# Kernel tuning notes

Measured on AMD Instinct MI355X. Metric: run time of the kernel, lower is better.

Reference implementation:

```python
import jax, jax.numpy as jnp
import numpy as np

VOCAB = 10000
EMBED = 512
HIDDEN = 1024
FEAT = 2048
PAD_IDX = 0


def setup_inputs() -> dict:
    key = jax.random.key(0)
    ks = jax.random.split(key, 12)
    s = lambda fan_in: 1.0 / np.sqrt(fan_in)
    features = jax.random.normal(ks[0], (64, FEAT), dtype=jnp.float32)
    captions = jax.random.randint(ks[1], (64, 32), 0, VOCAB)
    embed_table = jax.random.normal(ks[2], (VOCAB, EMBED), dtype=jnp.float32) * 0.02
    embed_table = embed_table.at[PAD_IDX].set(0.0)  # padding_idx row is zero
    W_init_h = jax.random.uniform(ks[3], (HIDDEN, FEAT), jnp.float32, -s(FEAT), s(FEAT))
    b_init_h = jnp.zeros((HIDDEN,), jnp.float32)
    W_init_c = jax.random.uniform(ks[4], (HIDDEN, FEAT), jnp.float32, -s(FEAT), s(FEAT))
    b_init_c = jnp.zeros((HIDDEN,), jnp.float32)
    W_ih = jax.random.uniform(ks[5], (4 * HIDDEN, EMBED), jnp.float32, -s(HIDDEN), s(HIDDEN))
    b_ih = jax.random.uniform(ks[6], (4 * HIDDEN,), jnp.float32, -s(HIDDEN), s(HIDDEN))
    W_hh = jax.random.uniform(ks[7], (4 * HIDDEN, HIDDEN), jnp.float32, -s(HIDDEN), s(HIDDEN))
    b_hh = jax.random.uniform(ks[8], (4 * HIDDEN,), jnp.float32, -s(HIDDEN), s(HIDDEN))
    W_fc = jax.random.uniform(ks[9], (VOCAB, HIDDEN), jnp.float32, -s(HIDDEN), s(HIDDEN))
    b_fc = jax.random.uniform(ks[10], (VOCAB,), jnp.float32, -s(HIDDEN), s(HIDDEN))
    return {
        "features": features, "captions": captions, "embed_table": embed_table,
        "W_init_h": W_init_h, "b_init_h": b_init_h, "W_init_c": W_init_c, "b_init_c": b_init_c,
        "W_ih": W_ih, "b_ih": b_ih, "W_hh": W_hh, "b_hh": b_hh,
        "W_fc": W_fc, "b_fc": b_fc,
    }


def _lstm_cell(x, h, c, W_ih, b_ih, W_hh, b_hh):
    # torch LSTMCell gate order: i, f, g, o
    gates = x @ W_ih.T + b_ih + h @ W_hh.T + b_hh  # [B, 4H]
    i, f, g, o = jnp.split(gates, 4, axis=-1)
    i = jax.nn.sigmoid(i)
    f = jax.nn.sigmoid(f)
    g = jnp.tanh(g)
    o = jax.nn.sigmoid(o)
    c = f * c + i * g
    h = o * jnp.tanh(c)
    return h, c


def reference(features, captions, embed_table, W_init_h, b_init_h, W_init_c, b_init_c,
              W_ih, b_ih, W_hh, b_hh, W_fc, b_fc):
    h0 = features @ W_init_h.T + b_init_h  # [B, H]
    c0 = features @ W_init_c.T + b_init_c  # [B, H]
    emb = embed_table[captions]            # [B, T, E]
    emb_t = jnp.swapaxes(emb, 0, 1)        # [T, B, E] for scan over time

    def step(carry, x_t):
        h, c = carry
        h, c = _lstm_cell(x_t, h, c, W_ih, b_ih, W_hh, b_hh)
        out = jax.nn.sigmoid(h @ W_fc.T + b_fc)  # [B, V]
        return (h, c), out

    _, outs = jax.lax.scan(step, (h0, c0), emb_t)
    return outs  # [T, B, V] matching torch.stack(dim=0)
```

## Files before the change

### kernel.cpp

```cpp
#include <hip/hip_runtime.h>


#define B_  64
#define T_  32
#define E_  512
#define H_  1024
#define V_  10000
#define F_  2048

typedef short short8 __attribute__((ext_vector_type(8)));
typedef float floatx4 __attribute__((ext_vector_type(4)));

__device__ __forceinline__ float bf2f(unsigned short u) {
  union { unsigned int i; float f; } c; c.i = ((unsigned int)u) << 16; return c.f;
}
__device__ __forceinline__ unsigned short f2bf(float f) {
  union { float f; unsigned int i; } c; c.f = f;
  unsigned int x = c.i;
  return (unsigned short)((x + 0x7fffu + ((x >> 16) & 1u)) >> 16);
}
__device__ __forceinline__ float sigmoidf_(float x) {
  return 1.0f / (1.0f + __expf(-x));
}
__device__ __forceinline__ void gl_lds16(const unsigned short* g, unsigned short* l) {
  __builtin_amdgcn_global_load_lds(
      (const __attribute__((address_space(1))) unsigned int*)g,
      (__attribute__((address_space(3))) unsigned int*)l, 16, 0, 0);
}
__device__ __forceinline__ int xcd_swz(int lin, int nwg) {
  if (nwg < 8) return lin;
  int q = nwg >> 3, r = nwg & 7;
  int xcd = lin & 7, pos = lin >> 3;
  return (xcd < r ? xcd * (q + 1) : r * (q + 1) + (xcd - r) * q) + pos;
}

#define C_WIH  524288
#define C_WHH  1048576
#define C_WFC  2560000
#define C_WI0  524288
#define C_WC0  524288
#define C_FEA  32768
#define C_TOT  (C_WIH + C_WHH + C_WFC + C_WI0 + C_WC0 + C_FEA)
#define NFLAGW 4096

__global__ __launch_bounds__(256) void cvt_all(
    const float* __restrict__ s0, const float* __restrict__ s1,
    const float* __restrict__ s2, const float* __restrict__ s3,
    const float* __restrict__ s4, const float* __restrict__ s5,
    unsigned short* __restrict__ d0, unsigned short* __restrict__ d1,
    unsigned short* __restrict__ d2, unsigned short* __restrict__ d3,
    unsigned short* __restrict__ d4, unsigned short* __restrict__ d5,
    unsigned int* __restrict__ flags) {
  if (blockIdx.x == 0) {
    for (int w = threadIdx.x; w < NFLAGW; w += 256) flags[w] = 0u;
  }
  int i = blockIdx.x * blockDim.x + threadIdx.x;
  int stride = gridDim.x * blockDim.x;
  for (; i < C_TOT; i += stride) {
    const float* s; unsigned short* d; int j = i;
    if (j < C_WIH)            { s = s0; d = d0; }
    else if ((j -= C_WIH) < C_WHH) { s = s1; d = d1; }
    else if ((j -= C_WHH) < C_WFC) { s = s2; d = d2; }
    else if ((j -= C_WFC) < C_WI0) { s = s3; d = d3; }
    else if ((j -= C_WI0) < C_WC0) { s = s4; d = d4; }
    else { j -= C_WC0; s = s5; d = d5; }
    float4 v = ((const float4*)s)[j];
    ushort4 o;
    o.x = f2bf(v.x); o.y = f2bf(v.y); o.z = f2bf(v.z); o.w = f2bf(v.w);
    ((ushort4*)d)[j] = o;
  }
}

__global__ __launch_bounds__(128) void embed_gather(
    const float* __restrict__ table, const int* __restrict__ captions,
    unsigned short* __restrict__ out) {
  int row = blockIdx.x;
  int t = row >> 6, b = row & 63;
  int idx = captions[b * T_ + t];
  const float4* src = (const float4*)(table + (size_t)idx * E_);
  ushort4* dst = (ushort4*)(out + (size_t)row * E_);
  for (int e = threadIdx.x; e < E_ / 4; e += blockDim.x) {
    float4 v = src[e];
    ushort4 o;
    o.x = f2bf(v.x); o.y = f2bf(v.y); o.z = f2bf(v.z); o.w = f2bf(v.w);
    dst[e] = o;
  }
}

template <int ACT_SIGMOID, int OUT_BF16, int OUT_INIT>
__global__ __launch_bounds__(256) void mfma_gemm128(
    const unsigned short* __restrict__ A, const unsigned short* __restrict__ W,
    const float* __restrict__ bias1, const float* __restrict__ bias2,
    void* __restrict__ out, void* __restrict__ out2, int M, int N, int K) {
  __shared__ unsigned short At[2][128 * 32];
  __shared__ unsigned short Wt[2][128 * 32];

  const int tid  = threadIdx.x;
  const int lane = tid & 63;
  const int wave = tid >> 6;
  const int l15  = lane & 15;
  const int quad = lane >> 4;
  const int wm   = (wave >> 1) * 64;
  const int wn   = (wave & 1) * 64;

  const int gx  = gridDim.x;
  const int nwg = gx * gridDim.y;
  const int wg  = xcd_swz(blockIdx.y * gx + blockIdx.x, nwg);
  const int m0  = (wg % gx) * 128;
  const int n0  = (wg / gx) * 128;
  const int ksl = (quad ^ (l15 & 3)) * 8;

  const int c0i = tid, c1i = tid + 256;
  const int ar0 = c0i >> 2, ak0 = (((c0i & 3) ^ (ar0 & 3)) * 8);
  const int ar1 = c1i >> 2, ak1 = (((c1i & 3) ^ (ar1 & 3)) * 8);
  int am0 = m0 + ar0; if (am0 > M - 1) am0 = M - 1;
  int am1 = m0 + ar1; if (am1 > M - 1) am1 = M - 1;
  int wn0 = n0 + ar0; if (wn0 > N - 1) wn0 = N - 1;
  int wn1 = n0 + ar1; if (wn1 > N - 1) wn1 = N - 1;
  const unsigned short* Ag0 = A + (size_t)am0 * K + ak0;
  const unsigned short* Ag1 = A + (size_t)am1 * K + ak1;
  const unsigned short* Wg0 = W + (size_t)wn0 * K + ak0;
  const unsigned short* Wg1 = W + (size_t)wn1 * K + ak1;

  floatx4 acc[4][4];
#pragma unroll
  for (int i = 0; i < 4; ++i)
#pragma unroll
    for (int j = 0; j < 4; ++j) acc[i][j] = (floatx4){0.f, 0.f, 0.f, 0.f};

  gl_lds16(Ag0, &At[0][c0i * 8]);
  gl_lds16(Ag1, &At[0][c1i * 8]);
  gl_lds16(Wg0, &Wt[0][c0i * 8]);
  gl_lds16(Wg1, &Wt[0][c1i * 8]);
  __syncthreads();

  int cur = 0;
  for (int k0 = 0; k0 < K; k0 += 32) {
    const int kn = k0 + 32;
    if (kn < K) {
      const int nb = cur ^ 1;
      gl_lds16(Ag0 + kn, &At[nb][c0i * 8]);
      gl_lds16(Ag1 + kn, &At[nb][c1i * 8]);
      gl_lds16(Wg0 + kn, &Wt[nb][c0i * 8]);
      gl_lds16(Wg1 + kn, &Wt[nb][c1i * 8]);
    }
    short8 a[4], b[4];
#pragma unroll
    for (int mt = 0; mt < 4; ++mt)
      a[mt] = *(const short8*)&At[cur][(wm + mt * 16 + l15) * 32 + ksl];
#pragma unroll
    for (int nt = 0; nt < 4; ++nt)
      b[nt] = *(const short8*)&Wt[cur][(wn + nt * 16 + l15) * 32 + ksl];
#pragma unroll
    for (int mt = 0; mt < 4; ++mt)
#pragma unroll
      for (int nt = 0; nt < 4; ++nt)
        acc[mt][nt] = __builtin_amdgcn_mfma_f32_16x16x32_bf16(a[mt], b[nt], acc[mt][nt], 0, 0, 0);
    __syncthreads();
    cur ^= 1;
  }

#pragma unroll
  for (int nt = 0; nt < 4; ++nt) {
    int col = n0 + wn + nt * 16 + l15;
    if (col >= N) continue;
    float bsum;
    if (OUT_INIT)
      bsum = (col < H_) ? bias1[col] : bias2[col - H_];
    else
      bsum = (bias1 ? bias1[col] : 0.f) + (bias2 ? bias2[col] : 0.f);
#pragma unroll
    for (int mt = 0; mt < 4; ++mt) {
#pragma unroll
      for (int r = 0; r < 4; ++r) {
        int m = m0 + wm + mt * 16 + quad * 4 + r;
        if (m >= M) continue;
        float v = acc[mt][nt][r] + bsum;
        if (ACT_SIGMOID) v = sigmoidf_(v);
        if (OUT_INIT) {
          if (col < H_)
            ((unsigned short*)out)[(size_t)m * H_ + col] = f2bf(v);
          else
            ((float*)out2)[(size_t)m * H_ + (col - H_)] = v;
        } else if (OUT_BF16) {
          ((unsigned short*)out)[(size_t)m * N + col] = f2bf(v);
        } else {
          ((float*)out)[(size_t)m * N + col] = v;
        }
      }
    }
  }
}

#define WSPAD2 1032
__global__ __launch_bounds__(512, 2) void lstm_persistent(
    const unsigned short* __restrict__ W_hh_b,
    const unsigned short* __restrict__ gx_b,
    const float* __restrict__ c0_f32,
    unsigned short* __restrict__ h_all,
    unsigned int* __restrict__ flags) {
  __shared__ unsigned short Ws[32 * WSPAD2];
  __shared__ float gbuf[4][32][33];

  const int tid  = threadIdx.x;
  const int lane = tid & 63;
  const int wave = tid >> 6;
  const int l15  = lane & 15;
  const int quad = lane >> 4;
  const int kb   = quad * 8;
  const int bid  = blockIdx.x;
  const int cg   = bid >> 1;
  const int bh   = bid & 1;
  const int colbase = cg * 8;
  const int kq   = wave >> 1;
  const int mt   = wave & 1;

#pragma unroll
  for (int it = 0; it < 8; ++it) {
    int u = wave * 8 + it;
    int n = u >> 1, half = u & 1;
    int grow = (n >> 3) * H_ + colbase + (n & 7);
    gl_lds16(W_hh_b + (size_t)grow * H_ + half * 512 + lane * 8,
             &Ws[n * WSPAD2 + half * 512]);
  }

  const int bq = tid >> 2;
  const int cp = tid & 3;
  const int gb = bh * 32 + bq;
  float cA = 0.f, cB = 0.f;
  if (tid < 128) {
    float2 cv = *(const float2*)(c0_f32 + (size_t)gb * H_ + colbase + 2 * cp);
    cA = cv.x; cB = cv.y;
  }

  const unsigned short* hbase =
      h_all + (size_t)(bh * 32 + mt * 16 + l15) * H_ + kq * 256 + kb;
  const unsigned short* wb0 = &Ws[(size_t)(l15)      * WSPAD2 + kq * 256 + kb];
  const unsigned short* wb1 = &Ws[(size_t)(16 + l15) * WSPAD2 + kq * 256 + kb];
  const unsigned int* pfw = flags + (size_t)(kq * 64 + 2 * (lane & 31) + bh);

  __syncthreads();

  for (int t = 0; t < T_; ++t) {
    unsigned int ui = 0, uf = 0, ug = 0, uo = 0;
    if (tid < 128) {
      const unsigned short* gxp =
          gx_b + (size_t)t * (B_ * 4 * H_) + (size_t)gb * (4 * H_) + colbase + 2 * cp;
      ui = *(const unsigned int*)(gxp + 0 * H_);
      uf = *(const unsigned int*)(gxp + 1 * H_);
      ug = *(const unsigned int*)(gxp + 2 * H_);
      uo = *(const unsigned int*)(gxp + 3 * H_);
    }

    if (t > 0) {
      const unsigned int tgt = (unsigned int)t;
      for (;;) {
        unsigned int v;
        asm volatile("global_load_dword %0, %1, off sc0 sc1"
                     : "=v"(v) : "v"(pfw) : "memory");
        asm volatile("s_waitcnt vmcnt(0)" ::: "memory");
        if (__all(v >= tgt)) break;
        __builtin_amdgcn_s_sleep(1);
      }
    }

    const unsigned short* hp = hbase + (size_t)t * (B_ * H_);
    short8 hx[8];
#pragma unroll
    for (int i = 0; i < 8; ++i)
      asm volatile("global_load_dwordx4 %0, %1, off sc0 sc1"
                   : "=v"(hx[i]) : "v"(hp + i * 32) : "memory");
    asm volatile("s_waitcnt vmcnt(0)" ::: "memory");
    __builtin_amdgcn_sched_barrier(0);

    floatx4 A0 = (floatx4){0.f, 0.f, 0.f, 0.f}, A1 = A0;
#pragma unroll
    for (int i = 0; i < 8; ++i) {
      short8 w0 = *(const short8*)(wb0 + i * 32);
      short8 w1 = *(const short8*)(wb1 + i * 32);
      A0 = __builtin_amdgcn_mfma_f32_16x16x32_bf16(hx[i], w0, A0, 0, 0, 0);
      A1 = __builtin_amdgcn_mfma_f32_16x16x32_bf16(hx[i], w1, A1, 0, 0, 0);
    }
#pragma unroll
    for (int r = 0; r < 4; ++r) {
      gbuf[kq][mt * 16 + quad * 4 + r][l15]      = A0[r];
      gbuf[kq][mt * 16 + quad * 4 + r][16 + l15] = A1[r];
    }
    __syncthreads();

    if (tid < 128) {
      const int c0c = 2 * cp, c1c = 2 * cp + 1;
      float giA = gbuf[0][bq][ 0 + c0c] + gbuf[1][bq][ 0 + c0c]
                + gbuf[2][bq][ 0 + c0c] + gbuf[3][bq][ 0 + c0c] + bf2f((unsigned short)(ui & 0xffff));
      float gfA = gbuf[0][bq][ 8 + c0c] + gbuf[1][bq][ 8 + c0c]
                + gbuf[2][bq][ 8 + c0c] + gbuf[3][bq][ 8 + c0c] + bf2f((unsigned short)(uf & 0xffff));
      float ggA = gbuf[0][bq][16 + c0c] + gbuf[1][bq][16 + c0c]
                + gbuf[2][bq][16 + c0c] + gbuf[3][bq][16 + c0c] + bf2f((unsigned short)(ug & 0xffff));
      float goA = gbuf[0][bq][24 + c0c] + gbuf[1][bq][24 + c0c]
                + gbuf[2][bq][24 + c0c] + gbuf[3][bq][24 + c0c] + bf2f((unsigned short)(uo & 0xffff));
      float giB = gbuf[0][bq][ 0 + c1c] + gbuf[1][bq][ 0 + c1c]
                + gbuf[2][bq][ 0 + c1c] + gbuf[3][bq][ 0 + c1c] + bf2f((unsigned short)(ui >> 16));
      float gfB = gbuf[0][bq][ 8 + c1c] + gbuf[1][bq][ 8 + c1c]
                + gbuf[2][bq][ 8 + c1c] + gbuf[3][bq][ 8 + c1c] + bf2f((unsigned short)(uf >> 16));
      float ggB = gbuf[0][bq][16 + c1c] + gbuf[1][bq][16 + c1c]
                + gbuf[2][bq][16 + c1c] + gbuf[3][bq][16 + c1c] + bf2f((unsigned short)(ug >> 16));
      float goB = gbuf[0][bq][24 + c1c] + gbuf[1][bq][24 + c1c]
                + gbuf[2][bq][24 + c1c] + gbuf[3][bq][24 + c1c] + bf2f((unsigned short)(uo >> 16));
      giA = sigmoidf_(giA); gfA = sigmoidf_(gfA); ggA = tanhf(ggA); goA = sigmoidf_(goA);
      giB = sigmoidf_(giB); gfB = sigmoidf_(gfB); ggB = tanhf(ggB); goB = sigmoidf_(goB);
      cA = gfA * cA + giA * ggA;
      cB = gfB * cB + giB * ggB;
      float hA = goA * tanhf(cA);
      float hB = goB * tanhf(cB);
      unsigned int hv = (unsigned int)f2bf(hA) | ((unsigned int)f2bf(hB) << 16);
      unsigned int* hop = (unsigned int*)(h_all + (size_t)(t + 1) * (B_ * H_)
                                          + (size_t)gb * H_ + colbase + 2 * cp);
      asm volatile("global_store_dword %0, %1, off sc0 sc1"
                   :: "v"(hop), "v"(hv) : "memory");
      asm volatile("s_waitcnt vmcnt(0)" ::: "memory");
    }

    if (t < T_ - 1) {
      __syncthreads();
      if (tid == 0) {
        const unsigned int tgt = (unsigned int)(t + 1);
        unsigned int* myf = flags + bid;
        asm volatile("global_store_dword %0, %1, off sc0 sc1"
                     :: "v"(myf), "v"(tgt) : "memory");
      }
    }
  }
}

extern "C" void kernel_launch(void* const* d_in, const int* in_sizes, int n_in,
                              void* d_out, int out_size, void* d_ws, size_t ws_size,
                              hipStream_t stream) {
  const float* features    = (const float*)d_in[0];
  const int*   captions    = (const int*)d_in[1];
  const float* embed_table = (const float*)d_in[2];
  const float* W_init_h    = (const float*)d_in[3];
  const float* b_init_h    = (const float*)d_in[4];
  const float* W_init_c    = (const float*)d_in[5];
  const float* b_init_c    = (const float*)d_in[6];
  const float* W_ih        = (const float*)d_in[7];
  const float* b_ih        = (const float*)d_in[8];
  const float* W_hh        = (const float*)d_in[9];
  const float* b_hh        = (const float*)d_in[10];
  const float* W_fc        = (const float*)d_in[11];
  const float* b_fc        = (const float*)d_in[12];
  float* out = (float*)d_out;

  char* ws = (char*)d_ws;
  auto alloc = [&](size_t bytes) -> char* {
    char* p = ws;
    ws += (bytes + 255) & ~(size_t)255;
    return p;
  };
  unsigned short* W_ih_b  = (unsigned short*)alloc((size_t)4 * H_ * E_ * 2);
  unsigned short* W_hh_b  = (unsigned short*)alloc((size_t)4 * H_ * H_ * 2);
  unsigned short* W_fc_b  = (unsigned short*)alloc((size_t)V_ * H_ * 2);
  unsigned short* Wih0_b  = (unsigned short*)alloc((size_t)H_ * F_ * 2);
  unsigned short* Wic0_b  = (unsigned short*)alloc((size_t)H_ * F_ * 2);
  unsigned short* feat_b  = (unsigned short*)alloc((size_t)B_ * F_ * 2);
  unsigned short* emb_b   = (unsigned short*)alloc((size_t)T_ * B_ * E_ * 2);
  unsigned short* gx_b    = (unsigned short*)alloc((size_t)T_ * B_ * 4 * H_ * 2);
  unsigned short* h_all   = (unsigned short*)alloc((size_t)(T_ + 1) * B_ * H_ * 2);
  float*          c_f32   = (float*)alloc((size_t)B_ * H_ * 4);
  unsigned int*   flags   = (unsigned int*)alloc((size_t)NFLAGW * 4);
  (void)ws_size; (void)in_sizes; (void)n_in; (void)out_size; (void)Wic0_b;

  hipLaunchKernelGGL(cvt_all, dim3(4096), dim3(256), 0, stream,
                     W_ih, W_hh, W_fc, W_init_h, W_init_c, features,
                     W_ih_b, W_hh_b, W_fc_b, Wih0_b, Wic0_b, feat_b, flags);

  hipLaunchKernelGGL(embed_gather, dim3(T_ * B_), dim3(128), 0, stream,
                     embed_table, captions, emb_b);

  hipLaunchKernelGGL((mfma_gemm128<0, 1, 1>), dim3(1, 2 * H_ / 128), dim3(256), 0, stream,
                     feat_b, Wih0_b, b_init_h, b_init_c,
                     (void*)h_all, (void*)c_f32, B_, 2 * H_, F_);

  hipLaunchKernelGGL((mfma_gemm128<0, 1, 0>), dim3(T_ * B_ / 128, 4 * H_ / 128), dim3(256), 0, stream,
                     emb_b, W_ih_b, b_ih, b_hh, (void*)gx_b, (void*)nullptr,
                     T_ * B_, 4 * H_, E_);

  hipLaunchKernelGGL(lstm_persistent, dim3(2 * H_ / 8), dim3(512), 0, stream,
                     W_hh_b, gx_b, c_f32, h_all, flags);

  hipLaunchKernelGGL((mfma_gemm128<1, 0, 0>), dim3(T_ * B_ / 128, (V_ + 127) / 128), dim3(256), 0, stream,
                     h_all + (size_t)B_ * H_, W_fc_b, b_fc, (const float*)nullptr,
                     (void*)out, (void*)nullptr, T_ * B_, V_, H_);
}
```

Baseline: 539.8 us.

## Fuse LSTM recurrence and output projection into one persistent producer/consumer kernel

Replaces the persistent LSTM kernel plus the separate FC GEMM with one 256-block kernel. 128 blocks run the recurrence, each covering all 64 batch rows for 8 hidden columns, so 128 blocks instead of 256 take part in each step's grid barrier. The other 128 blocks keep a swizzled 79-row slice of W_fc in LDS and compute sigmoid(h_t·W_fc^T+b) for each step once the flags show h_t is ready, overlapping the vocabulary projection with the recurrence. Flags are padded to 16-word strides and all blocks poll all 128 flags. The trade-offs are a large LDS footprint, heavy reliance on all 256 blocks being co-resident, and FC work limited to 4 waves per block.

```diff
diff --git a/kernel.cpp b/kernel.cpp
--- a/kernel.cpp
+++ b/kernel.cpp
@@ -193,140 +193,225 @@
 }
 
 #define WSPAD2 1032
-__global__ __launch_bounds__(512, 2) void lstm_persistent(
+#define SMEMB  161792
+__global__ __launch_bounds__(512, 2) void lstm_fused(
     const unsigned short* __restrict__ W_hh_b,
     const unsigned short* __restrict__ gx_b,
     const float* __restrict__ c0_f32,
     unsigned short* __restrict__ h_all,
-    unsigned int* __restrict__ flags) {
-  __shared__ unsigned short Ws[32 * WSPAD2];
-  __shared__ float gbuf[4][32][33];
+    unsigned int* __restrict__ flags,
+    const unsigned short* __restrict__ W_fc_b,
+    const float* __restrict__ b_fc,
+    float* __restrict__ out) {
+  __shared__ __align__(16) unsigned char smem[SMEMB];
 
   const int tid  = threadIdx.x;
   const int lane = tid & 63;
   const int wave = tid >> 6;
   const int l15  = lane & 15;
   const int quad = lane >> 4;
-  const int kb   = quad * 8;
   const int bid  = blockIdx.x;
-  const int cg   = bid >> 1;
-  const int bh   = bid & 1;
-  const int colbase = cg * 8;
-  const int kq   = wave >> 1;
-  const int mt   = wave & 1;
-
-#pragma unroll
-  for (int it = 0; it < 8; ++it) {
-    int u = wave * 8 + it;
-    int n = u >> 1, half = u & 1;
-    int grow = (n >> 3) * H_ + colbase + (n & 7);
-    gl_lds16(W_hh_b + (size_t)grow * H_ + half * 512 + lane * 8,
-             &Ws[n * WSPAD2 + half * 512]);
-  }
-
-  const int bq = tid >> 2;
-  const int cp = tid & 3;
-  const int gb = bh * 32 + bq;
-  float cA = 0.f, cB = 0.f;
-  if (tid < 128) {
-    float2 cv = *(const float2*)(c0_f32 + (size_t)gb * H_ + colbase + 2 * cp);
-    cA = cv.x; cB = cv.y;
-  }
-
-  const unsigned short* hbase =
-      h_all + (size_t)(bh * 32 + mt * 16 + l15) * H_ + kq * 256 + kb;
-  const unsigned short* wb0 = &Ws[(size_t)(l15)      * WSPAD2 + kq * 256 + kb];
-  const unsigned short* wb1 = &Ws[(size_t)(16 + l15) * WSPAD2 + kq * 256 + kb];
-  const unsigned int* pfw = flags + (size_t)(kq * 64 + 2 * (lane & 31) + bh);
-
+  const unsigned int* pf0 = flags + (size_t)(lane)      * 16;
+  const unsigned int* pf1 = flags + (size_t)(lane + 64) * 16;
+
+  if (bid < 128) {
+    unsigned short* Ws = (unsigned short*)smem;
+    float (*gbuf)[64][33] = (float (*)[64][33])(smem + 66048);
+    const int colbase = bid * 8;
+    const int kb  = quad * 8;
+    const int kq  = wave >> 1;
+    const int bf0 = (wave & 1) * 2;
+    const int bf1 = bf0 + 1;
+
+#pragma unroll
+    for (int it = 0; it < 8; ++it) {
+      int u = wave * 8 + it;
+      int n = u >> 1, half = u & 1;
+      int grow = (n >> 3) * H_ + colbase + (n & 7);
+      gl_lds16(W_hh_b + (size_t)grow * H_ + half * 512 + lane * 8,
+               &Ws[n * WSPAD2 + half * 512]);
+    }
+
+    const int cb = tid >> 2;
+    const int cp = tid & 3;
+    float cA = 0.f, cB = 0.f;
+    if (tid < 256) {
+      float2 cv = *(const float2*)(c0_f32 + (size_t)cb * H_ + colbase + 2 * cp);
+      cA = cv.x; cB = cv.y;
+    }
+
+    const unsigned short* hb0 = h_all + (size_t)(bf0 * 16 + l15) * H_ + kq * 256 + kb;
+    const unsigned short* hb1 = h_all + (size_t)(bf1 * 16 + l15) * H_ + kq * 256 + kb;
+    const unsigned short* wb0 = &Ws[(size_t)(l15)      * WSPAD2 + kq * 256 + kb];
+    const unsigned short* wb1 = &Ws[(size_t)(16 + l15) * WSPAD2 + kq * 256 + kb];
+
+    __syncthreads();
+
+    for (int t = 0; t < T_; ++t) {
+      unsigned int ui = 0, uf = 0, ug = 0, uo = 0;
+      if (tid < 256) {
+        const unsigned short* gxp =
+            gx_b + (size_t)t * (B_ * 4 * H_) + (size_t)cb * (4 * H_) + colbase + 2 * cp;
+        ui = *(const unsigned int*)(gxp + 0 * H_);
+        uf = *(const unsigned int*)(gxp + 1 * H_);
+        ug = *(const unsigned int*)(gxp + 2 * H_);
+        uo = *(const unsigned int*)(gxp + 3 * H_);
+      }
+
+      const size_t toff = (size_t)t * (B_ * H_);
+      short8 hx0[8], hx1[8];
+#pragma unroll
+      for (int i = 0; i < 8; ++i) {
+        asm volatile("global_load_dwordx4 %0, %1, off sc0 sc1"
+                     : "=v"(hx0[i]) : "v"(hb0 + toff + i * 32) : "memory");
+        asm volatile("global_load_dwordx4 %0, %1, off sc0 sc1"
+                     : "=v"(hx1[i]) : "v"(hb1 + toff + i * 32) : "memory");
+      }
+      asm volatile("s_waitcnt vmcnt(0)" ::: "memory");
+      __builtin_amdgcn_sched_barrier(0);
+
+      floatx4 A0 = (floatx4){0.f,0.f,0.f,0.f}, A1 = A0, B0 = A0, B1 = A0;
+#pragma unroll
+      for (int i = 0; i < 8; ++i) {
+        short8 w0 = *(const short8*)(wb0 + i * 32);
+        short8 w1 = *(const short8*)(wb1 + i * 32);
+        A0 = __builtin_amdgcn_mfma_f32_16x16x32_bf16(hx0[i], w0, A0, 0, 0, 0);
+        A1 = __builtin_amdgcn_mfma_f32_16x16x32_bf16(hx0[i], w1, A1, 0, 0, 0);
+        B0 = __builtin_amdgcn_mfma_f32_16x16x32_bf16(hx1[i], w0, B0, 0, 0, 0);
+        B1 = __builtin_amdgcn_mfma_f32_16x16x32_bf16(hx1[i], w1, B1, 0, 0, 0);
+      }
+#pragma unroll
+      for (int r = 0; r < 4; ++r) {
+        gbuf[kq][bf0 * 16 + quad * 4 + r][l15]      = A0[r];
+        gbuf[kq][bf0 * 16 + quad * 4 + r][16 + l15] = A1[r];
+        gbuf[kq][bf1 * 16 + quad * 4 + r][l15]      = B0[r];
+        gbuf[kq][bf1 * 16 + quad * 4 + r][16 + l15] = B1[r];
+      }
+      __syncthreads();
+
+      if (tid < 256) {
+        const int c0c = 2 * cp, c1c = 2 * cp + 1;
+        float giA = gbuf[0][cb][ 0 + c0c] + gbuf[1][cb][ 0 + c0c]
+                  + gbuf[2][cb][ 0 + c0c] + gbuf[3][cb][ 0 + c0c] + bf2f((unsigned short)(ui & 0xffff));
+        float gfA = gbuf[0][cb][ 8 + c0c] + gbuf[1][cb][ 8 + c0c]
+                  + gbuf[2][cb][ 8 + c0c] + gbuf[3][cb][ 8 + c0c] + bf2f((unsigned short)(uf & 0xffff));
+        float ggA = gbuf[0][cb][16 + c0c] + gbuf[1][cb][16 + c0c]
+                  + gbuf[2][cb][16 + c0c] + gbuf[3][cb][16 + c0c] + bf2f((unsigned short)(ug & 0xffff));
+        float goA = gbuf[0][cb][24 + c0c] + gbuf[1][cb][24 + c0c]
+                  + gbuf[2][cb][24 + c0c] + gbuf[3][cb][24 + c0c] + bf2f((unsigned short)(uo & 0xffff));
+        float giB = gbuf[0][cb][ 0 + c1c] + gbuf[1][cb][ 0 + c1c]
+                  + gbuf[2][cb][ 0 + c1c] + gbuf[3][cb][ 0 + c1c] + bf2f((unsigned short)(ui >> 16));
+        float gfB = gbuf[0][cb][ 8 + c1c] + gbuf[1][cb][ 8 + c1c]
+                  + gbuf[2][cb][ 8 + c1c] + gbuf[3][cb][ 8 + c1c] + bf2f((unsigned short)(uf >> 16));
+        float ggB = gbuf[0][cb][16 + c1c] + gbuf[1][cb][16 + c1c]
+                  + gbuf[2][cb][16 + c1c] + gbuf[3][cb][16 + c1c] + bf2f((unsigned short)(ug >> 16));
+        float goB = gbuf[0][cb][24 + c1c] + gbuf[1][cb][24 + c1c]
+                  + gbuf[2][cb][24 + c1c] + gbuf[3][cb][24 + c1c] + bf2f((unsigned short)(uo >> 16));
+        giA = sigmoidf_(giA); gfA = sigmoidf_(gfA); ggA = tanhf(ggA); goA = sigmoidf_(goA);
+        giB = sigmoidf_(giB); gfB = sigmoidf_(gfB); ggB = tanhf(ggB); goB = sigmoidf_(goB);
+        cA = gfA * cA + giA * ggA;
+        cB = gfB * cB + giB * ggB;
+        float hA = goA * tanhf(cA);
+        float hB = goB * tanhf(cB);
+        unsigned int hv = (unsigned int)f2bf(hA) | ((unsigned int)f2bf(hB) << 16);
+        unsigned int* hop = (unsigned int*)(h_all + (size_t)(t + 1) * (B_ * H_)
+                                            + (size_t)cb * H_ + colbase + 2 * cp);
+        asm volatile("global_store_dword %0, %1, off sc0 sc1"
+                     :: "v"(hop), "v"(hv) : "memory");
+        asm volatile("s_waitcnt vmcnt(0)" ::: "memory");
+      }
+
+      __syncthreads();
+      if (tid == 0) {
+        const unsigned int tg = (unsigned int)(t + 1);
+        unsigned int* myf = flags + (size_t)bid * 16;
+        asm volatile("global_store_dword %0, %1, off sc0 sc1"
+                     :: "v"(myf), "v"(tg) : "memory");
+      }
+      if (t < T_ - 1 && wave == 0) {
+        const unsigned int tgt = (unsigned int)(t + 1);
+        for (;;) {
+          unsigned int v0, v1;
+          asm volatile("global_load_dword %0, %1, off sc0 sc1"
+                       : "=v"(v0) : "v"(pf0) : "memory");
+          asm volatile("global_load_dword %0, %1, off sc0 sc1"
+                       : "=v"(v1) : "v"(pf1) : "memory");
+          asm volatile("s_waitcnt vmcnt(0)" ::: "memory");
+          if (__all(v0 >= tgt && v1 >= tgt)) break;
+          __builtin_amdgcn_s_sleep(1);
+        }
+      }
+      __syncthreads();
+    }
+    return;
+  }
+
+  const int f  = bid - 128;
+  const int vb = f * 79;
+  for (int it = 0; it < 20; ++it) {
+    int u = wave * 20 + it;
+    if (u < 158) {
+      int r = u >> 1, half = u & 1;
+      int vr = vb + r; if (vr > V_ - 1) vr = V_ - 1;
+      int gchunk = (half * 64 + lane) ^ (r & 7);
+      gl_lds16(W_fc_b + (size_t)vr * H_ + (size_t)gchunk * 8,
+               (unsigned short*)(smem + (size_t)r * 2048 + half * 1024));
+    }
+  }
   __syncthreads();
 
-  for (int t = 0; t < T_; ++t) {
-    unsigned int ui = 0, uf = 0, ug = 0, uo = 0;
-    if (tid < 128) {
-      const unsigned short* gxp =
-          gx_b + (size_t)t * (B_ * 4 * H_) + (size_t)gb * (4 * H_) + colbase + 2 * cp;
-      ui = *(const unsigned int*)(gxp + 0 * H_);
-      uf = *(const unsigned int*)(gxp + 1 * H_);
-      ug = *(const unsigned int*)(gxp + 2 * H_);
-      uo = *(const unsigned int*)(gxp + 3 * H_);
-    }
-
-    if (t > 0) {
+  for (int t = 1; t <= T_; ++t) {
+    if (wave == 0) {
       const unsigned int tgt = (unsigned int)t;
       for (;;) {
-        unsigned int v;
+        unsigned int v0, v1;
         asm volatile("global_load_dword %0, %1, off sc0 sc1"
-                     : "=v"(v) : "v"(pfw) : "memory");
+                     : "=v"(v0) : "v"(pf0) : "memory");
+        asm volatile("global_load_dword %0, %1, off sc0 sc1"
+                     : "=v"(v1) : "v"(pf1) : "memory");
         asm volatile("s_waitcnt vmcnt(0)" ::: "memory");
-        if (__all(v >= tgt)) break;
+        if (__all(v0 >= tgt && v1 >= tgt)) break;
         __builtin_amdgcn_s_sleep(1);
       }
     }
-
-    const unsigned short* hp = hbase + (size_t)t * (B_ * H_);
-    short8 hx[8];
-#pragma unroll
-    for (int i = 0; i < 8; ++i)
-      asm volatile("global_load_dwordx4 %0, %1, off sc0 sc1"
-                   : "=v"(hx[i]) : "v"(hp + i * 32) : "memory");
-    asm volatile("s_waitcnt vmcnt(0)" ::: "memory");
-    __builtin_amdgcn_sched_barrier(0);
-
-    floatx4 A0 = (floatx4){0.f, 0.f, 0.f, 0.f}, A1 = A0;
-#pragma unroll
-    for (int i = 0; i < 8; ++i) {
-      short8 w0 = *(const short8*)(wb0 + i * 32);
-      short8 w1 = *(const short8*)(wb1 + i * 32);
-      A0 = __builtin_amdgcn_mfma_f32_16x16x32_bf16(hx[i], w0, A0, 0, 0, 0);
-      A1 = __builtin_amdgcn_mfma_f32_16x16x32_bf16(hx[i], w1, A1, 0, 0, 0);
-    }
-#pragma unroll
-    for (int r = 0; r < 4; ++r) {
-      gbuf[kq][mt * 16 + quad * 4 + r][l15]      = A0[r];
-      gbuf[kq][mt * 16 + quad * 4 + r][16 + l15] = A1[r];
-    }
     __syncthreads();
 
-    if (tid < 128) {
-      const int c0c = 2 * cp, c1c = 2 * cp + 1;
-      float giA = gbuf[0][bq][ 0 + c0c] + gbuf[1][bq][ 0 + c0c]
-                + gbuf[2][bq][ 0 + c0c] + gbuf[3][bq][ 0 + c0c] + bf2f((unsigned short)(ui & 0xffff));
-      float gfA = gbuf[0][bq][ 8 + c0c] + gbuf[1][bq][ 8 + c0c]
-                + gbuf[2][bq][ 8 + c0c] + gbuf[3][bq][ 8 + c0c] + bf2f((unsigned short)(uf & 0xffff));
-      float ggA = gbuf[0][bq][16 + c0c] + gbuf[1][bq][16 + c0c]
-                + gbuf[2][bq][16 + c0c] + gbuf[3][bq][16 + c0c] + bf2f((unsigned short)(ug & 0xffff));
-      float goA = gbuf[0][bq][24 + c0c] + gbuf[1][bq][24 + c0c]
-                + gbuf[2][bq][24 + c0c] + gbuf[3][bq][24 + c0c] + bf2f((unsigned short)(uo & 0xffff));
-      float giB = gbuf[0][bq][ 0 + c1c] + gbuf[1][bq][ 0 + c1c]
-                + gbuf[2][bq][ 0 + c1c] + gbuf[3][bq][ 0 + c1c] + bf2f((unsigned short)(ui >> 16));
-      float gfB = gbuf[0][bq][ 8 + c1c] + gbuf[1][bq][ 8 + c1c]
-                + gbuf[2][bq][ 8 + c1c] + gbuf[3][bq][ 8 + c1c] + bf2f((unsigned short)(uf >> 16));
-      float ggB = gbuf[0][bq][16 + c1c] + gbuf[1][bq][16 + c1c]
-                + gbuf[2][bq][16 + c1c] + gbuf[3][bq][16 + c1c] + bf2f((unsigned short)(ug >> 16));
-      float goB = gbuf[0][bq][24 + c1c] + gbuf[1][bq][24 + c1c]
-                + gbuf[2][bq][24 + c1c] + gbuf[3][bq][24 + c1c] + bf2f((unsigned short)(uo >> 16));
-      giA = sigmoidf_(giA); gfA = sigmoidf_(gfA); ggA = tanhf(ggA); goA = sigmoidf_(goA);
-      giB = sigmoidf_(giB); gfB = sigmoidf_(gfB); ggB = tanhf(ggB); goB = sigmoidf_(goB);
-      cA = gfA * cA + giA * ggA;
-      cB = gfB * cB + giB * ggB;
-      float hA = goA * tanhf(cA);
-      float hB = goB * tanhf(cB);
-      unsigned int hv = (unsigned int)f2bf(hA) | ((unsigned int)f2bf(hB) << 16);
-      unsigned int* hop = (unsigned int*)(h_all + (size_t)(t + 1) * (B_ * H_)
-                                          + (size_t)gb * H_ + colbase + 2 * cp);
-      asm volatile("global_store_dword %0, %1, off sc0 sc1"
-                   :: "v"(hop), "v"(hv) : "memory");
-      asm volatile("s_waitcnt vmcnt(0)" ::: "memory");
-    }
-
-    if (t < T_ - 1) {
-      __syncthreads();
-      if (tid == 0) {
-        const unsigned int tgt = (unsigned int)(t + 1);
-        unsigned int* myf = flags + bid;
-        asm volatile("global_store_dword %0, %1, off sc0 sc1"
-                     :: "v"(myf), "v"(tgt) : "memory");
+    if (wave >= 1 && wave <= 4) {
+      const int bf = wave - 1;
+      const unsigned short* ap =
+          h_all + (size_t)t * (B_ * H_) + (size_t)(bf * 16 + l15) * H_ + quad * 8;
+      float* orow = out + (size_t)(t - 1) * (B_ * V_);
+      floatx4 acc[5];
+#pragma unroll
+      for (int c = 0; c < 5; ++c) acc[c] = (floatx4){0.f, 0.f, 0.f, 0.f};
+      const unsigned char* lb[5];
+      int sw[5];
+#pragma unroll
+      for (int c = 0; c < 5; ++c) {
+        int lrow = c * 16 + l15;
+        lb[c] = smem + (size_t)lrow * 2048;
+        sw[c] = lrow & 7;
+      }
+#pragma unroll 4
+      for (int i = 0; i < 32; ++i) {
+        short8 a = *(const short8*)(ap + i * 32);
+        const int ch = quad + i * 4;
+#pragma unroll
+        for (int c = 0; c < 5; ++c) {
+          short8 b = *(const short8*)(lb[c] + ((ch ^ sw[c]) << 4));
+          acc[c] = __builtin_amdgcn_mfma_f32_16x16x32_bf16(a, b, acc[c], 0, 0, 0);
+        }
+      }
+#pragma unroll
+      for (int c = 0; c < 5; ++c) {
+        const int lcol = c * 16 + l15;
+        const int col  = vb + lcol;
+        if (lcol < 79 && col < V_) {
+          const float bs = b_fc[col];
+#pragma unroll
+          for (int r = 0; r < 4; ++r)
+            orow[(size_t)(bf * 16 + quad * 4 + r) * V_ + col] = sigmoidf_(acc[c][r] + bs);
+        }
       }
     }
   }
@@ -384,10 +469,6 @@
                      emb_b, W_ih_b, b_ih, b_hh, (void*)gx_b, (void*)nullptr,
                      T_ * B_, 4 * H_, E_);
 
-  hipLaunchKernelGGL(lstm_persistent, dim3(2 * H_ / 8), dim3(512), 0, stream,
-                     W_hh_b, gx_b, c_f32, h_all, flags);
-
-  hipLaunchKernelGGL((mfma_gemm128<1, 0, 0>), dim3(T_ * B_ / 128, (V_ + 127) / 128), dim3(256), 0, stream,
-                     h_all + (size_t)B_ * H_, W_fc_b, b_fc, (const float*)nullptr,
-                     (void*)out, (void*)nullptr, T_ * B_, V_, H_);
-}
+  hipLaunchKernelGGL(lstm_fused, dim3(256), dim3(512), 0, stream,
+                     W_hh_b, gx_b, c_f32, h_all, flags, W_fc_b, b_fc, out);
+}
```

Result: faster. 511.6 us (-5.2%).
